# Kernel optimization log

Hardware: AMD Instinct MI355X
Metric: run time of the kernel (lower is better)

## Reference

```python
import jax, jax.numpy as jnp
import numpy as np

E = 11        # number of language experts
ALPHA = 1000.0  # soft-argmax temperature
C1 = 8.0      # gate sharpness


def setup_inputs() -> dict:
    key = jax.random.key(0)
    ks = jax.random.split(key, 6)
    B, S, H, L = 16, 256, 1024, 32
    return {
        "transformer_out": jax.random.normal(ks[0], (B, S, H), dtype=jnp.float32),
        "logits_ld": jax.random.normal(ks[1], (B, E), dtype=jnp.float32),
        "W1": jax.random.normal(ks[2], (E, H, H), dtype=jnp.float32) * 0.02,
        "b1": jax.random.normal(ks[3], (E, H), dtype=jnp.float32) * 0.02,
        "W2": jax.random.normal(ks[4], (E, H, L), dtype=jnp.float32) * 0.02,
        "b2": jax.random.normal(ks[5], (E, L), dtype=jnp.float32) * 0.02,
    }


def reference(transformer_out, logits_ld, W1, b1, W2, b2):
    # soft argmax over language-detect logits -> continuous lang id per sample [B]
    sm = jax.nn.softmax(logits_ld * ALPHA, axis=1)
    lang_id = jnp.sum(sm * jnp.arange(logits_ld.shape[1], dtype=logits_ld.dtype), axis=1)

    # soft top-hat gate per expert i: sigmoid((id-(i-.5))*c1)*sigmoid(((i+.5)-id)*c1) -> [E,B]
    idx = jnp.arange(E, dtype=lang_id.dtype)[:, None]          # [E,1]
    gate = (jax.nn.sigmoid((lang_id[None, :] - (idx - 0.5)) * C1)
            * jax.nn.sigmoid((idx + 0.5 - lang_id[None, :]) * C1))  # [E,B]

    # all 11 expert FFN branches as batched GEMMs (dropout = identity in eval)
    h = jax.nn.relu(jnp.einsum('bsh,ehd->ebsd', transformer_out, W1)
                    + b1[:, None, None, :])                     # [E,B,S,H]
    t = jnp.einsum('ebsd,edl->ebsl', h, W2) + b2[:, None, None, :]  # [E,B,S,L]

    # gate per (expert, batch) and sum over experts -> [B,S,L]
    logits = jnp.einsum('ebsl,eb->bsl', t, gate)
    return logits
```

## Files before the change

### kernel.cpp

```cpp
#include <hip/hip_runtime.h>
#include <hip/hip_bf16.h>
#include <stdint.h>

#define E_ 11
#define B_ 16
#define S_ 256
#define H_ 1024
#define L_ 32
#define GEPS 1e-4f

typedef __attribute__((ext_vector_type(8))) short short8;
typedef __attribute__((ext_vector_type(4))) float f32x4;

__device__ __forceinline__ unsigned short f2bf(float f) {
  unsigned u = __float_as_uint(f);
  unsigned r = (u + 0x7FFFu + ((u >> 16) & 1u)) >> 16;
  return (unsigned short)r;
}
__device__ __forceinline__ float bf2f(unsigned short v) {
  return __uint_as_float(((unsigned)v) << 16);
}
__device__ __forceinline__ void gload_lds16(const void* g, void* l) {
  __builtin_amdgcn_global_load_lds(
      (const __attribute__((address_space(1))) unsigned int*)g,
      (__attribute__((address_space(3))) unsigned int*)l, 16, 0, 0);
}
__device__ __forceinline__ float sigf(float x) { return 1.0f / (1.0f + expf(-x)); }

__device__ __forceinline__ float lang_of(const float* __restrict__ logits, int b) {
  float lv[E_];
  float m = -1e30f;
  #pragma unroll
  for (int i = 0; i < E_; ++i) { lv[i] = logits[b * E_ + i]; m = fmaxf(m, lv[i]); }
  float den = 0.f, num = 0.f;
  #pragma unroll
  for (int i = 0; i < E_; ++i) {
    float z = expf((lv[i] - m) * 1000.0f);
    den += z; num += z * (float)i;
  }
  return num / den;
}
__device__ __forceinline__ float gate_of(float lang, int e) {
  float fe = (float)e;
  return sigf((lang - (fe - 0.5f)) * 8.0f) * sigf(((fe + 0.5f) - lang) * 8.0f);
}

__device__ __forceinline__ bool expert_active(const float* __restrict__ logits, int e) {
  int b = threadIdx.x & 15;
  float lang = lang_of(logits, b);
  unsigned long long m = __ballot(fabsf(lang - (float)e) < 1.7f);
  return m != 0ull;
}

__global__ __launch_bounds__(256) void prep_kernel(
    const float* __restrict__ x, const float* __restrict__ logits,
    const float* __restrict__ W1, const float* __restrict__ W2,
    unsigned short* __restrict__ xbf, unsigned short* __restrict__ W1T,
    unsigned short* __restrict__ W2T, int* __restrict__ plan) {
  int bid = blockIdx.x;
  int tid = threadIdx.x;
  __shared__ float t[64][65];

  if (bid < 2048) {
    int i = (bid * 256 + tid) * 8;
    float4 f0 = *(const float4*)(x + i);
    float4 f1 = *(const float4*)(x + i + 4);
    short8 o;
    o[0] = (short)f2bf(f0.x); o[1] = (short)f2bf(f0.y);
    o[2] = (short)f2bf(f0.z); o[3] = (short)f2bf(f0.w);
    o[4] = (short)f2bf(f1.x); o[5] = (short)f2bf(f1.y);
    o[6] = (short)f2bf(f1.z); o[7] = (short)f2bf(f1.w);
    *(short8*)(xbf + i) = o;
    return;
  }
  if (bid < 2048 + 2816) {
    int tt = bid - 2048;
    int e = tt >> 8, rest = tt & 255;
    int k0 = (rest >> 4) * 64, d0 = (rest & 15) * 64;
    if (!expert_active(logits, e)) return;
    int kr = tid >> 2, dc = (tid & 3) * 16;
    const float* src = W1 + ((size_t)e << 20) + (size_t)(k0 + kr) * H_ + d0 + dc;
    #pragma unroll
    for (int q = 0; q < 4; ++q) {
      float4 v = *(const float4*)(src + q * 4);
      t[kr][dc + q * 4 + 0] = v.x; t[kr][dc + q * 4 + 1] = v.y;
      t[kr][dc + q * 4 + 2] = v.z; t[kr][dc + q * 4 + 3] = v.w;
    }
    __syncthreads();
    int dr = tid >> 2, kc = (tid & 3) * 16;
    short8 v0, v1;
    #pragma unroll
    for (int j = 0; j < 8; ++j) v0[j] = (short)f2bf(t[kc + j][dr]);
    #pragma unroll
    for (int j = 0; j < 8; ++j) v1[j] = (short)f2bf(t[kc + 8 + j][dr]);
    unsigned short* dst = W1T + ((size_t)e << 20) + (size_t)(d0 + dr) * H_ + k0 + kc;
    *(short8*)(dst) = v0;
    *(short8*)(dst + 8) = v1;
    return;
  }
  if (bid < 2048 + 2816 + 176) {
    int tt = bid - 4864;
    int e = tt >> 4, k0 = (tt & 15) * 64;
    if (!expert_active(logits, e)) return;
    int kr = tid >> 2, lc = (tid & 3) * 8;
    const float* src = W2 + (size_t)e * H_ * L_ + (size_t)(k0 + kr) * L_ + lc;
    float4 a = *(const float4*)(src);
    float4 b = *(const float4*)(src + 4);
    t[kr][lc + 0] = a.x; t[kr][lc + 1] = a.y; t[kr][lc + 2] = a.z; t[kr][lc + 3] = a.w;
    t[kr][lc + 4] = b.x; t[kr][lc + 5] = b.y; t[kr][lc + 6] = b.z; t[kr][lc + 7] = b.w;
    __syncthreads();
    int lr = tid >> 3, kc = (tid & 7) * 8;
    short8 v;
    #pragma unroll
    for (int j = 0; j < 8; ++j) v[j] = (short)f2bf(t[kc + j][lr]);
    *(short8*)(W2T + (size_t)(e * L_ + lr) * H_ + k0 + kc) = v;
    return;
  }
  {
    __shared__ float langs[16];
    __shared__ int wcnt[4];
    if (tid < 16) langs[tid] = lang_of(logits, tid);
    __syncthreads();
    bool act = false;
    if (tid < E_ * B_) {
      int e = tid >> 4, b = tid & 15;
      act = gate_of(langs[b], e) >= GEPS;
    }
    unsigned long long m = __ballot(act);
    int w = tid >> 6;
    if ((tid & 63) == 0) wcnt[w] = __popcll(m);
    __syncthreads();
    int off = 0;
    for (int i = 0; i < w; ++i) off += wcnt[i];
    int rank = __popcll(m & ((1ull << (tid & 63)) - 1ull));
    if (act) plan[1 + off + rank] = tid;
    if (tid == 0) plan[0] = wcnt[0] + wcnt[1] + wcnt[2] + wcnt[3];
  }
}

#define WAITV(N) asm volatile("s_waitcnt vmcnt(" #N ")" ::: "memory")

__global__ __launch_bounds__(512, 2) void ffn_kernel(
    const unsigned short* __restrict__ xbf, const unsigned short* __restrict__ W1T,
    const unsigned short* __restrict__ W2T, const float* __restrict__ b1,
    const float* __restrict__ b2, const float* __restrict__ logits,
    const int* __restrict__ plan, float* __restrict__ out) {
  int bid = blockIdx.x;
  int cnt = plan[0];
  if (bid >= (cnt << 2)) return;
  int pair = plan[1 + (bid >> 2)];
  int dt = bid & 3;
  int e = pair >> 4, b = pair & 15;
  float g = gate_of(lang_of(logits, b), e);

  __shared__ __align__(16) char smem[98304];

  int tid = threadIdx.x;
  int w = tid >> 6, wr = w >> 1, wc = w & 1;
  int l = tid & 63, l15 = l & 15, l4 = l >> 4;

  const unsigned short* gA[2]; int ldsA[2];
  const unsigned short* gB[2]; int ldsB[2];
  #pragma unroll
  for (int jj = 0; jj < 2; ++jj) {
    int c = jj * 512 + tid;
    int p = c >> 3, uu = (c & 7) ^ (p & 7);
    int row = p * 2 + (uu >> 2), kc = (uu & 3) * 8;
    gA[jj] = xbf + (size_t)(b * S_ + row) * H_ + kc;
    ldsA[jj] = c * 16;
    gB[jj] = W1T + ((size_t)e * H_ + dt * 256 + row) * H_ + kc;
    ldsB[jj] = 16384 + c * 16;
  }
  int offA[4], offB[8];
  #pragma unroll
  for (int mf = 0; mf < 4; ++mf) {
    int row = wr * 64 + mf * 16 + l15;
    int p = row >> 1;
    int slot = (((row & 1) * 4) + l4) ^ (p & 7);
    offA[mf] = p * 128 + slot * 16;
  }
  #pragma unroll
  for (int nf = 0; nf < 8; ++nf) {
    int d = wc * 128 + nf * 16 + l15;
    int p = d >> 1;
    int slot = (((d & 1) * 4) + l4) ^ (p & 7);
    offB[nf] = 16384 + p * 128 + slot * 16;
  }

  f32x4 acc[4][8];
  #pragma unroll
  for (int mf = 0; mf < 4; ++mf)
    #pragma unroll
    for (int nf = 0; nf < 8; ++nf) acc[mf][nf] = f32x4{0.f, 0.f, 0.f, 0.f};

  auto stage = [&](int buf, int kt) {
    int bb = buf * 32768;
    int ko = kt * 32;
    gload_lds16(gA[0] + ko, smem + bb + ldsA[0]);
    gload_lds16(gA[1] + ko, smem + bb + ldsA[1]);
    gload_lds16(gB[0] + ko, smem + bb + ldsB[0]);
    gload_lds16(gB[1] + ko, smem + bb + ldsB[1]);
  };

  stage(0, 0);
  stage(1, 1);
  WAITV(4);
  __builtin_amdgcn_s_barrier();

  #pragma unroll
  for (int kt = 0; kt < 32; ++kt) {
    if (kt < 30) stage((kt + 2) % 3, kt + 2);
    int bb = (kt % 3) * 32768;
    short8 af[4], bf[8];
    #pragma unroll
    for (int mf = 0; mf < 4; ++mf) af[mf] = *(const short8*)(smem + bb + offA[mf]);
    #pragma unroll
    for (int nf = 0; nf < 8; ++nf) bf[nf] = *(const short8*)(smem + bb + offB[nf]);
    #pragma unroll
    for (int mf = 0; mf < 4; ++mf)
      #pragma unroll
      for (int nf = 0; nf < 8; ++nf)
        acc[mf][nf] =
            __builtin_amdgcn_mfma_f32_16x16x32_bf16(af[mf], bf[nf], acc[mf][nf], 0, 0, 0);
    if (kt < 31) {
      if (kt < 30) { WAITV(4); }
      else { WAITV(0); }
      __builtin_amdgcn_s_barrier();
    }
  }

  __syncthreads();

  float b1v[8];
  #pragma unroll
  for (int nf = 0; nf < 8; ++nf)
    b1v[nf] = b1[e * H_ + dt * 256 + wc * 128 + nf * 16 + l15];

  char* P = smem + w * 8192;
  f32x4 tacc[4][2];
  #pragma unroll
  for (int mf = 0; mf < 4; ++mf)
    #pragma unroll
    for (int nl = 0; nl < 2; ++nl) tacc[mf][nl] = f32x4{0.f, 0.f, 0.f, 0.f};

  #pragma unroll
  for (int half = 0; half < 2; ++half) {
    #pragma unroll
    for (int mf = 0; mf < 4; ++mf)
      #pragma unroll
      for (int nfh = 0; nfh < 4; ++nfh) {
        int nf = half * 4 + nfh;
        #pragma unroll
        for (int rr = 0; rr < 4; ++rr) {
          int row = mf * 16 + l4 * 4 + rr;
          int col = nfh * 16 + l15;
          float v = fmaxf(acc[mf][nf][rr] + b1v[nf], 0.f);
          *(unsigned short*)(P + row * 128 + (((col >> 3) ^ (row & 7)) * 16) +
                             (col & 7) * 2) = f2bf(v);
        }
      }
    #pragma unroll
    for (int kk = 0; kk < 2; ++kk) {
      short8 ap[4], bw[2];
      #pragma unroll
      for (int mf = 0; mf < 4; ++mf) {
        int row = mf * 16 + l15;
        int ch = kk * 4 + l4;
        ap[mf] = *(const short8*)(P + row * 128 + ((ch ^ (row & 7)) * 16));
      }
      #pragma unroll
      for (int nl = 0; nl < 2; ++nl)
        bw[nl] = *(const short8*)(W2T + (size_t)(e * L_ + nl * 16 + l15) * H_ +
                                  dt * 256 + wc * 128 + half * 64 + kk * 32 + l4 * 8);
      #pragma unroll
      for (int mf = 0; mf < 4; ++mf)
        #pragma unroll
        for (int nl = 0; nl < 2; ++nl)
          tacc[mf][nl] =
              __builtin_amdgcn_mfma_f32_16x16x32_bf16(ap[mf], bw[nl], tacc[mf][nl], 0, 0, 0);
    }
  }

  float* Tr = (float*)smem + w * 2048;
  #pragma unroll
  for (int mf = 0; mf < 4; ++mf)
    #pragma unroll
    for (int nl = 0; nl < 2; ++nl)
      #pragma unroll
      for (int rr = 0; rr < 4; ++rr) {
        int row = mf * 16 + l4 * 4 + rr;
        int col = nl * 16 + l15;
        Tr[row * 32 + col] = tacc[mf][nl][rr];
      }
  __syncthreads();
  float* Tb = (float*)smem;
  #pragma unroll
  for (int jj = 0; jj < 16; ++jj) {
    int ei = tid + jj * 512;
    int srow = ei >> 5, lcol = ei & 31;
    int wr2 = srow >> 6, r6 = srow & 63;
    float sum = Tb[(wr2 * 2 + 0) * 2048 + r6 * 32 + lcol] +
                Tb[(wr2 * 2 + 1) * 2048 + r6 * 32 + lcol];
    if (dt == 0) sum += b2[e * L_ + lcol];
    atomicAdd(out + (size_t)(b * S_ + srow) * L_ + lcol, g * sum);
  }
}

__global__ void fb_kernel(const float* __restrict__ x, const float* __restrict__ logits,
                          const float* __restrict__ W1, const float* __restrict__ b1,
                          const float* __restrict__ W2, const float* __restrict__ b2,
                          float* __restrict__ out) {
  int bid = blockIdx.x;
  int e = bid >> 9;
  int r = bid & 511;
  int b = r >> 5, st = r & 31, s0 = st * 8;
  float g = gate_of(lang_of(logits, b), e);
  if (g < GEPS) return;

  __shared__ float xs[8][H_];
  __shared__ unsigned short hs[8][H_];
  int tid = threadIdx.x;
  for (int jj = 0; jj < 32; ++jj) {
    int idx = tid + jj * 256;
    int s = idx >> 10, k = idx & 1023;
    xs[s][k] = x[(size_t)(b * S_ + s0 + s) * H_ + k];
  }
  __syncthreads();
  for (int qq = 0; qq < 4; ++qq) {
    int d = tid + qq * 256;
    float a[8];
    #pragma unroll
    for (int s = 0; s < 8; ++s) a[s] = 0.f;
    for (int k = 0; k < H_; ++k) {
      float wv = W1[((size_t)e << 20) + (size_t)k * H_ + d];
      #pragma unroll
      for (int s = 0; s < 8; ++s) a[s] += xs[s][k] * wv;
    }
    float bv = b1[e * H_ + d];
    #pragma unroll
    for (int s = 0; s < 8; ++s) hs[s][d] = f2bf(fmaxf(a[s] + bv, 0.f));
  }
  __syncthreads();
  int s = tid >> 5, lcol = tid & 31;
  float acc = 0.f;
  for (int d = 0; d < H_; ++d)
    acc += bf2f(hs[s][d]) * W2[(size_t)(e * H_ + d) * L_ + lcol];
  acc += b2[e * L_ + lcol];
  atomicAdd(out + (size_t)(b * S_ + s0 + s) * L_ + lcol, g * acc);
}

extern "C" void kernel_launch(void* const* d_in, const int* in_sizes, int n_in,
                              void* d_out, int out_size, void* d_ws, size_t ws_size,
                              hipStream_t stream) {
  (void)in_sizes; (void)n_in;
  const float* x  = (const float*)d_in[0];
  const float* lg = (const float*)d_in[1];
  const float* W1 = (const float*)d_in[2];
  const float* b1 = (const float*)d_in[3];
  const float* W2 = (const float*)d_in[4];
  const float* b2 = (const float*)d_in[5];
  float* out = (float*)d_out;

  hipMemsetAsync(d_out, 0, (size_t)out_size * sizeof(float), stream);

  const size_t OFF_X = 0;
  const size_t OFF_W1 = OFF_X + 8388608;
  const size_t OFF_W2 = OFF_W1 + 23068672;
  const size_t OFF_PLAN = OFF_W2 + 720896;
  const size_t WS_NEED = OFF_PLAN + 1024;

  if (ws_size >= WS_NEED) {
    unsigned short* xbf = (unsigned short*)((char*)d_ws + OFF_X);
    unsigned short* W1T = (unsigned short*)((char*)d_ws + OFF_W1);
    unsigned short* W2T = (unsigned short*)((char*)d_ws + OFF_W2);
    int* plan = (int*)((char*)d_ws + OFF_PLAN);
    prep_kernel<<<2048 + 2816 + 176 + 1, 256, 0, stream>>>(x, lg, W1, W2, xbf, W1T, W2T, plan);
    ffn_kernel<<<704, 512, 0, stream>>>(xbf, W1T, W2T, b1, b2, lg, plan, out);
  } else {
    fb_kernel<<<E_ * B_ * (S_ / 8), 256, 0, stream>>>(x, lg, W1, b1, W2, b2, out);
  }
}
```

Baseline: 61.09 us.

## Split GEMM main loop into two half-phases with interleaved loads and setprio

Restructures the K-loop of the first expert GEMM into two phases, each loading half of the B fragments from LDS and issuing half of the global-to-LDS prefetch before its MFMA block. The phases are separated by extra barriers, and each MFMA block runs under s_setprio(1). The goal is to overlap LDS reads and global prefetch with matrix work across waves, in a ping-pong style. In exchange it adds four barriers per iteration, which could cost synchronisation overhead, and the wait placement becomes harder to reason about.

Measured after the change: 62.79 us. 1.03x slower.

```diff
diff --git a/kernel.cpp b/kernel.cpp
--- a/kernel.cpp
+++ b/kernel.cpp
@@ -193,40 +193,61 @@
     #pragma unroll
     for (int nf = 0; nf < 8; ++nf) acc[mf][nf] = f32x4{0.f, 0.f, 0.f, 0.f};
 
-  auto stage = [&](int buf, int kt) {
-    int bb = buf * 32768;
-    int ko = kt * 32;
+  auto stageA = [&](int buf, int kt) {
+    int bb = buf * 32768, ko = kt * 32;
     gload_lds16(gA[0] + ko, smem + bb + ldsA[0]);
     gload_lds16(gA[1] + ko, smem + bb + ldsA[1]);
+  };
+  auto stageB = [&](int buf, int kt) {
+    int bb = buf * 32768, ko = kt * 32;
     gload_lds16(gB[0] + ko, smem + bb + ldsB[0]);
     gload_lds16(gB[1] + ko, smem + bb + ldsB[1]);
   };
 
-  stage(0, 0);
-  stage(1, 1);
+  stageA(0, 0); stageB(0, 0);
+  stageA(1, 1); stageB(1, 1);
   WAITV(4);
   __builtin_amdgcn_s_barrier();
 
   #pragma unroll
   for (int kt = 0; kt < 32; ++kt) {
-    if (kt < 30) stage((kt + 2) % 3, kt + 2);
     int bb = (kt % 3) * 32768;
-    short8 af[4], bf[8];
+    short8 af[4], bfA[4];
     #pragma unroll
     for (int mf = 0; mf < 4; ++mf) af[mf] = *(const short8*)(smem + bb + offA[mf]);
     #pragma unroll
-    for (int nf = 0; nf < 8; ++nf) bf[nf] = *(const short8*)(smem + bb + offB[nf]);
+    for (int nf = 0; nf < 4; ++nf) bfA[nf] = *(const short8*)(smem + bb + offB[nf]);
+    if (kt < 30) stageA((kt + 2) % 3, kt + 2);
+    __builtin_amdgcn_s_barrier();
+    asm volatile("s_waitcnt lgkmcnt(0)" ::: "memory");
+    __builtin_amdgcn_sched_barrier(0);
+    __builtin_amdgcn_s_setprio(1);
     #pragma unroll
     for (int mf = 0; mf < 4; ++mf)
       #pragma unroll
-      for (int nf = 0; nf < 8; ++nf)
+      for (int nf = 0; nf < 4; ++nf)
         acc[mf][nf] =
-            __builtin_amdgcn_mfma_f32_16x16x32_bf16(af[mf], bf[nf], acc[mf][nf], 0, 0, 0);
-    if (kt < 31) {
-      if (kt < 30) { WAITV(4); }
-      else { WAITV(0); }
-      __builtin_amdgcn_s_barrier();
-    }
+            __builtin_amdgcn_mfma_f32_16x16x32_bf16(af[mf], bfA[nf], acc[mf][nf], 0, 0, 0);
+    __builtin_amdgcn_s_setprio(0);
+    __builtin_amdgcn_s_barrier();
+    short8 bfB[4];
+    #pragma unroll
+    for (int nf = 0; nf < 4; ++nf) bfB[nf] = *(const short8*)(smem + bb + offB[4 + nf]);
+    if (kt < 30) stageB((kt + 2) % 3, kt + 2);
+    if (kt < 30) { WAITV(4); }
+    else if (kt == 30) { WAITV(0); }
+    __builtin_amdgcn_s_barrier();
+    asm volatile("s_waitcnt lgkmcnt(0)" ::: "memory");
+    __builtin_amdgcn_sched_barrier(0);
+    __builtin_amdgcn_s_setprio(1);
+    #pragma unroll
+    for (int mf = 0; mf < 4; ++mf)
+      #pragma unroll
+      for (int nf = 0; nf < 4; ++nf)
+        acc[mf][4 + nf] =
+            __builtin_amdgcn_mfma_f32_16x16x32_bf16(af[mf], bfB[nf], acc[mf][4 + nf], 0, 0, 0);
+    __builtin_amdgcn_s_setprio(0);
+    __builtin_amdgcn_s_barrier();
   }
 
   __syncthreads();
```

## Fuse fp32-to-bf16 activation conversion into GEMM A-tile staging

Applied to the files above, without the earlier changes.

Removes the separate x-to-bf16 pass from the prep kernel. The FFN kernel now loads fp32 activations into registers one tile ahead, converts them with packed bf16 conversion instructions, and writes them to LDS itself. The W1 tiles still go through direct global-to-LDS loads. This saves the write and re-read of the 8 MB bf16 copy of x, but it doubles the A-operand global traffic per tile and re-reads the fp32 x from each of the 4 column blocks. It also adds register pressure and VGPR-routed stores to the main loop, and the wait counts had to be retuned.

After: 71.96 us. 17.8% more time.

```diff
diff --git a/kernel.cpp b/kernel.cpp
--- a/kernel.cpp
+++ b/kernel.cpp
@@ -53,28 +53,16 @@
 }
 
 __global__ __launch_bounds__(256) void prep_kernel(
-    const float* __restrict__ x, const float* __restrict__ logits,
+    const float* __restrict__ logits,
     const float* __restrict__ W1, const float* __restrict__ W2,
-    unsigned short* __restrict__ xbf, unsigned short* __restrict__ W1T,
-    unsigned short* __restrict__ W2T, int* __restrict__ plan) {
+    unsigned short* __restrict__ W1T, unsigned short* __restrict__ W2T,
+    int* __restrict__ plan) {
   int bid = blockIdx.x;
   int tid = threadIdx.x;
   __shared__ float t[64][65];
 
-  if (bid < 2048) {
-    int i = (bid * 256 + tid) * 8;
-    float4 f0 = *(const float4*)(x + i);
-    float4 f1 = *(const float4*)(x + i + 4);
-    short8 o;
-    o[0] = (short)f2bf(f0.x); o[1] = (short)f2bf(f0.y);
-    o[2] = (short)f2bf(f0.z); o[3] = (short)f2bf(f0.w);
-    o[4] = (short)f2bf(f1.x); o[5] = (short)f2bf(f1.y);
-    o[6] = (short)f2bf(f1.z); o[7] = (short)f2bf(f1.w);
-    *(short8*)(xbf + i) = o;
-    return;
-  }
-  if (bid < 2048 + 2816) {
-    int tt = bid - 2048;
+  if (bid < 2816) {
+    int tt = bid;
     int e = tt >> 8, rest = tt & 255;
     int k0 = (rest >> 4) * 64, d0 = (rest & 15) * 64;
     if (!expert_active(logits, e)) return;
@@ -98,8 +86,8 @@
     *(short8*)(dst + 8) = v1;
     return;
   }
-  if (bid < 2048 + 2816 + 176) {
-    int tt = bid - 4864;
+  if (bid < 2816 + 176) {
+    int tt = bid - 2816;
     int e = tt >> 4, k0 = (tt & 15) * 64;
     if (!expert_active(logits, e)) return;
     int kr = tid >> 2, lc = (tid & 3) * 8;
@@ -138,10 +126,11 @@
   }
 }
 
-#define WAITV(N) asm volatile("s_waitcnt vmcnt(" #N ")" ::: "memory")
+#define SYNC_TILE(VM) \
+  asm volatile("s_waitcnt vmcnt(" #VM ") lgkmcnt(0)\n\ts_barrier" ::: "memory")
 
 __global__ __launch_bounds__(512, 2) void ffn_kernel(
-    const unsigned short* __restrict__ xbf, const unsigned short* __restrict__ W1T,
+    const float* __restrict__ x, const unsigned short* __restrict__ W1T,
     const unsigned short* __restrict__ W2T, const float* __restrict__ b1,
     const float* __restrict__ b2, const float* __restrict__ logits,
     const int* __restrict__ plan, float* __restrict__ out) {
@@ -159,14 +148,14 @@
   int w = tid >> 6, wr = w >> 1, wc = w & 1;
   int l = tid & 63, l15 = l & 15, l4 = l >> 4;
 
-  const unsigned short* gA[2]; int ldsA[2];
+  const float* gAf[2]; int ldsA[2];
   const unsigned short* gB[2]; int ldsB[2];
   #pragma unroll
   for (int jj = 0; jj < 2; ++jj) {
     int c = jj * 512 + tid;
     int p = c >> 3, uu = (c & 7) ^ (p & 7);
     int row = p * 2 + (uu >> 2), kc = (uu & 3) * 8;
-    gA[jj] = xbf + (size_t)(b * S_ + row) * H_ + kc;
+    gAf[jj] = x + (size_t)(b * S_ + row) * H_ + kc;
     ldsA[jj] = c * 16;
     gB[jj] = W1T + ((size_t)e * H_ + dt * 256 + row) * H_ + kc;
     ldsB[jj] = 16384 + c * 16;
@@ -193,23 +182,48 @@
     #pragma unroll
     for (int nf = 0; nf < 8; ++nf) acc[mf][nf] = f32x4{0.f, 0.f, 0.f, 0.f};
 
-  auto stage = [&](int buf, int kt) {
+  float4 ar[4];
+  auto ldA = [&](int kt) {
+    int ko = kt * 32;
+    ar[0] = *(const float4*)(gAf[0] + ko);
+    ar[1] = *(const float4*)(gAf[0] + ko + 4);
+    ar[2] = *(const float4*)(gAf[1] + ko);
+    ar[3] = *(const float4*)(gAf[1] + ko + 4);
+  };
+  auto cvtWriteA = [&](int buf) {
     int bb = buf * 32768;
-    int ko = kt * 32;
-    gload_lds16(gA[0] + ko, smem + bb + ldsA[0]);
-    gload_lds16(gA[1] + ko, smem + bb + ldsA[1]);
+    uint4 w0, w1;
+    asm("v_cvt_pk_bf16_f32 %0, %1, %2" : "=v"(w0.x) : "v"(ar[0].x), "v"(ar[0].y));
+    asm("v_cvt_pk_bf16_f32 %0, %1, %2" : "=v"(w0.y) : "v"(ar[0].z), "v"(ar[0].w));
+    asm("v_cvt_pk_bf16_f32 %0, %1, %2" : "=v"(w0.z) : "v"(ar[1].x), "v"(ar[1].y));
+    asm("v_cvt_pk_bf16_f32 %0, %1, %2" : "=v"(w0.w) : "v"(ar[1].z), "v"(ar[1].w));
+    asm("v_cvt_pk_bf16_f32 %0, %1, %2" : "=v"(w1.x) : "v"(ar[2].x), "v"(ar[2].y));
+    asm("v_cvt_pk_bf16_f32 %0, %1, %2" : "=v"(w1.y) : "v"(ar[2].z), "v"(ar[2].w));
+    asm("v_cvt_pk_bf16_f32 %0, %1, %2" : "=v"(w1.z) : "v"(ar[3].x), "v"(ar[3].y));
+    asm("v_cvt_pk_bf16_f32 %0, %1, %2" : "=v"(w1.w) : "v"(ar[3].z), "v"(ar[3].w));
+    *(uint4*)(smem + bb + ldsA[0]) = w0;
+    *(uint4*)(smem + bb + ldsA[1]) = w1;
+  };
+  auto stageB = [&](int buf, int kt) {
+    int bb = buf * 32768, ko = kt * 32;
     gload_lds16(gB[0] + ko, smem + bb + ldsB[0]);
     gload_lds16(gB[1] + ko, smem + bb + ldsB[1]);
   };
 
-  stage(0, 0);
-  stage(1, 1);
-  WAITV(4);
-  __builtin_amdgcn_s_barrier();
+  ldA(0); cvtWriteA(0);
+  ldA(1); cvtWriteA(1);
+  stageB(0, 0);
+  ldA(2);
+  __builtin_amdgcn_sched_barrier(0);
+  stageB(1, 1);
+  SYNC_TILE(6);
 
   #pragma unroll
   for (int kt = 0; kt < 32; ++kt) {
-    if (kt < 30) stage((kt + 2) % 3, kt + 2);
+    if (kt < 30) cvtWriteA((kt + 2) % 3);
+    if (kt < 29) ldA(kt + 3);
+    __builtin_amdgcn_sched_barrier(0);
+    if (kt < 30) stageB((kt + 2) % 3, kt + 2);
     int bb = (kt % 3) * 32768;
     short8 af[4], bf[8];
     #pragma unroll
@@ -222,10 +236,12 @@
       for (int nf = 0; nf < 8; ++nf)
         acc[mf][nf] =
             __builtin_amdgcn_mfma_f32_16x16x32_bf16(af[mf], bf[nf], acc[mf][nf], 0, 0, 0);
-    if (kt < 31) {
-      if (kt < 30) { WAITV(4); }
-      else { WAITV(0); }
-      __builtin_amdgcn_s_barrier();
+    if (kt < 29) {
+      SYNC_TILE(6);
+    } else if (kt == 29) {
+      SYNC_TILE(2);
+    } else if (kt == 30) {
+      SYNC_TILE(0);
     }
   }
 
@@ -363,19 +379,17 @@
 
   hipMemsetAsync(d_out, 0, (size_t)out_size * sizeof(float), stream);
 
-  const size_t OFF_X = 0;
-  const size_t OFF_W1 = OFF_X + 8388608;
+  const size_t OFF_W1 = 0;
   const size_t OFF_W2 = OFF_W1 + 23068672;
   const size_t OFF_PLAN = OFF_W2 + 720896;
   const size_t WS_NEED = OFF_PLAN + 1024;
 
   if (ws_size >= WS_NEED) {
-    unsigned short* xbf = (unsigned short*)((char*)d_ws + OFF_X);
     unsigned short* W1T = (unsigned short*)((char*)d_ws + OFF_W1);
     unsigned short* W2T = (unsigned short*)((char*)d_ws + OFF_W2);
     int* plan = (int*)((char*)d_ws + OFF_PLAN);
-    prep_kernel<<<2048 + 2816 + 176 + 1, 256, 0, stream>>>(x, lg, W1, W2, xbf, W1T, W2T, plan);
-    ffn_kernel<<<704, 512, 0, stream>>>(xbf, W1T, W2T, b1, b2, lg, plan, out);
+    prep_kernel<<<2816 + 176 + 1, 256, 0, stream>>>(lg, W1, W2, W1T, W2T, plan);
+    ffn_kernel<<<704, 512, 0, stream>>>(x, W1T, W2T, b1, b2, lg, plan, out);
   } else {
     fb_kernel<<<E_ * B_ * (S_ / 8), 256, 0, stream>>>(x, lg, W1, b1, W2, b2, out);
   }
```
